# Optimization experiments

Measured on AMD Instinct MI355X. Metric: run time of the kernel, lower is better.

## Reference

```python
import jax, jax.numpy as jnp
import numpy as np

N_NODES = 100000
N_EDGES = 800000
VOCAB = 256      # node_dict_size
NODE_DIM = 256
HIDDEN = 256
N_MASK = 10000


def setup_inputs() -> dict:
    key = jax.random.key(0)
    ks = jax.random.split(key, 8)
    return {
        "x": jax.random.randint(ks[0], (N_NODES, 1), 0, VOCAB, dtype=jnp.int64 if jax.config.jax_enable_x64 else jnp.int32),
        "edge_index": jax.random.randint(ks[1], (2, N_EDGES), 0, N_NODES, dtype=jnp.int32),
        "mask_x_position": jax.random.randint(ks[2], (N_MASK,), 0, N_NODES, dtype=jnp.int32),
        "emb": jax.random.normal(ks[3], (VOCAB, NODE_DIM), dtype=jnp.float32) * (NODE_DIM ** -0.5),
        "W1": jax.random.normal(ks[4], (NODE_DIM, HIDDEN), dtype=jnp.float32) * (NODE_DIM ** -0.5),
        "b1": jnp.zeros((HIDDEN,), dtype=jnp.float32),
        "W2": jax.random.normal(ks[5], (HIDDEN, VOCAB), dtype=jnp.float32) * (HIDDEN ** -0.5),
        "b2": jnp.zeros((VOCAB,), dtype=jnp.float32),
    }


def _gcn_conv(h, W, b, src, dst, norm, n_nodes):
    # PyG GCNConv: out = scatter_add(norm * (h @ W)[src], dst) + b
    hw = h @ W                                      # [N, out]
    msgs = hw[src] * norm[:, None]                  # [E+N, out]
    out = jax.ops.segment_sum(msgs, dst, num_segments=n_nodes)
    return out + b


def _gcn_norm(edge_index, n_nodes):
    # add self-loops, compute sym-normalized edge weights (PyG gcn_norm)
    loops = jnp.arange(n_nodes, dtype=edge_index.dtype)
    src = jnp.concatenate([edge_index[0], loops])
    dst = jnp.concatenate([edge_index[1], loops])
    deg = jax.ops.segment_sum(jnp.ones_like(dst, dtype=jnp.float32), dst,
                              num_segments=n_nodes)  # in-degree incl. self-loop
    dinv = jnp.where(deg > 0, jax.lax.rsqrt(deg), 0.0)
    norm = dinv[src] * dinv[dst]                    # [E+N]
    return src, dst, norm


def reference(x, edge_index, mask_x_position, emb, W1, b1, W2, b2):
    n_nodes = x.shape[0]
    src, dst, norm = _gcn_norm(edge_index, n_nodes)
    h = emb[x[:, 0]]                                # Embedding + squeeze(1) -> [N, node_dim]
    # dropout p=0 / eval mode -> identity
    h = _gcn_conv(h, W1, b1, src, dst, norm, n_nodes)
    h = jax.nn.relu(h)
    h = _gcn_conv(h, W2, b2, src, dst, norm, n_nodes)  # [N, vocab]
    return jax.nn.log_softmax(h[mask_x_position], axis=1)
```

## Files before the change

kernel.cpp:

```cpp
#include <hip/hip_runtime.h>
#include <stdint.h>

#define NN 100000
#define NE 800000
#define ND 256
#define NM 10000
#define NMP 10048
#define NPB 256
#define NBK 391
#define BCAP 2560
#define TILE 4096
#define EBK ((NE + TILE - 1) / TILE)

typedef __attribute__((ext_vector_type(8))) short bf16x8;
typedef __attribute__((ext_vector_type(4))) float f32x4;

__device__ __forceinline__ float bf2f(unsigned short u) {
    return __uint_as_float(((unsigned)u) << 16);
}
__device__ __forceinline__ unsigned short f2bf(float f) {
    unsigned u = __float_as_uint(f);
    u += 0x7fffu + ((u >> 16) & 1u);
    return (unsigned short)(u >> 16);
}


__global__ void k_maskmap(const int* __restrict__ mpos, int* __restrict__ minfo,
                          unsigned char* __restrict__ mb, unsigned char* __restrict__ fb,
                          int* __restrict__ gcur, int* __restrict__ nctr) {
    int j = blockIdx.x * 256 + threadIdx.x;
    if (j < NM) {
        int p = mpos[j];
        minfo[p] = (j + 1) << 1;
        mb[p] = 1;
        fb[p] = 1;
    }
    if (j < NBK) gcur[j << 4] = j * BCAP;
    if (j == 0) *nctr = 0;
}

__global__ __launch_bounds__(256) void k_bin(
    const int* __restrict__ src, const int* __restrict__ dst,
    const unsigned char* __restrict__ mb, unsigned char* __restrict__ fb,
    int* __restrict__ gcur, int* __restrict__ ebuf,
    const float* __restrict__ emb, const float* __restrict__ W1,
    const float* __restrict__ W2,
    unsigned short* __restrict__ M1, unsigned short* __restrict__ W2t) {
    __shared__ int lcnt[NBK];
    __shared__ int sd[TILE], ss[TILE];
    __shared__ float er[ND];
    int b = blockIdx.x, t = threadIdx.x;
    if (b >= EBK) {
        int bb = b - EBK;
        if (bb < ND) {
            er[t] = emb[bb * ND + t];
            __syncthreads();
            float acc = 0.f;
            for (int k = 0; k < ND; k++) acc += er[k] * W1[k * ND + t];
            M1[bb * ND + t] = f2bf(acc);
        } else {
            int n = bb - ND;
            W2t[n * ND + t] = f2bf(W2[t * ND + n]);
        }
        return;
    }
    for (int i = t; i < NBK; i += 256) lcnt[i] = 0;
    __syncthreads();
    int e0 = b * TILE;
#pragma unroll
    for (int k = 0; k < TILE / 256; k++) {
        int idx = t + k * 256;
        int e = e0 + idx;
        if (e < NE) {
            int d = dst[e], s = src[e];
            sd[idx] = d; ss[idx] = s;
            atomicAdd(&lcnt[d >> 8], 1);
            if (mb[d] == 1) fb[s] = 1;
        }
    }
    __syncthreads();
    for (int i = t; i < NBK; i += 256) {
        int c = lcnt[i];
        lcnt[i] = c ? atomicAdd(&gcur[i << 4], c) : 0;
    }
    __syncthreads();
    int nv = min(NE - e0, TILE);
#pragma unroll
    for (int k = 0; k < TILE / 256; k++) {
        int idx = t + k * 256;
        if (idx < nv) {
            int d = sd[idx], s = ss[idx];
            int bk = d >> 8, j = d & 255;
            int pos = atomicAdd(&lcnt[bk], 1);
            if (pos < (bk + 1) * BCAP) ebuf[pos] = s | (j << 17);
        }
    }
}

__global__ void k_bhist(const int* __restrict__ gcur, const int* __restrict__ ebuf,
                        const int* __restrict__ x, const unsigned char* __restrict__ mb,
                        const unsigned char* __restrict__ fb,
                        int* __restrict__ carr, int4* __restrict__ xd4,
                        int* __restrict__ nctr, int* __restrict__ part) {
    __shared__ int bins[NPB];
    __shared__ int rs[4];
    int b = blockIdx.x, t = threadIdx.x;
    int lane = t & 63, wv = t >> 6;
    bins[t] = 0;
    __syncthreads();
    int n = min(gcur[b << 4] - b * BCAP, BCAP);
    int base = b * BCAP;
    for (int i = t; i < n; i += 256)
        atomicAdd(&bins[ebuf[base + i] >> 17], 1);
    __syncthreads();
    int node = b * NPB + t;
    int w = 0;
    if (node < NN) {
        int c = bins[t];
        carr[node] = c;
        float dv = rsqrtf((float)c + 1.0f);
        int cc = 0;
        if (fb[node] == 1) cc = atomicAdd(nctr, 1);
        xd4[node] = make_int4(x[node], __float_as_int(dv), cc, 0);
        w = c + ((mb[node] == 1) ? c : 0);
    }
#pragma unroll
    for (int o = 32; o >= 1; o >>= 1) w += __shfl_xor(w, o, 64);
    if (lane == 0) rs[wv] = w;
    __syncthreads();
    if (t == 0) part[b] = rs[0] + rs[1] + rs[2] + rs[3];
}

__global__ __launch_bounds__(256) void k_place(
    const int* __restrict__ gcur, const int* __restrict__ ebuf,
    const int* __restrict__ minfo, const unsigned char* __restrict__ fb,
    const int* __restrict__ carr, const int* __restrict__ part,
    const int4* __restrict__ xd4, int* __restrict__ off, int2* __restrict__ pairs,
    int4* __restrict__ nrec) {
    __shared__ int sinfo[NPB], lc1[NPB], lc2[NPB];
    __shared__ int bred[4], wtot[4];
    int b = blockIdx.x, t = threadIdx.x;
    int lane = t & 63, wv = t >> 6;
    int pv = 0;
    for (int i = t; i < b; i += 256) pv += part[i];
#pragma unroll
    for (int o = 32; o >= 1; o >>= 1) pv += __shfl_xor(pv, o, 64);
    if (lane == 0) bred[wv] = pv;
    __syncthreads();
    int pbase = bred[0] + bred[1] + bred[2] + bred[3];
    int node = b * NPB + t;
    int c = 0, m = 0, f = 0;
    if (node < NN) {
        c = carr[node];
        int mv = minfo[node];
        if (mv > 0) m = mv;
        f = (fb[node] == 1) ? 1 : 0;
    }
    int wgt = c + (m ? c : 0);
    int xx = wgt;
    for (int o = 1; o < 64; o <<= 1) { int y = __shfl_up(xx, o, 64); if (lane >= o) xx += y; }
    if (lane == 63) wtot[wv] = xx;
    __syncthreads();
    int wadd = 0;
#pragma unroll
    for (int k = 0; k < 4; k++) if (k < wv) wadd += wtot[k];
    int excl = xx - wgt + wadd;
    int myoff = pbase + excl;
    if (node < NN) {
        off[node] = myoff;
        if (f) {
            int4 xv = xd4[node];
            nrec[xv.z] = make_int4(xv.x, xv.y, myoff, c);
        }
    }
    sinfo[t] = m | f;
    lc1[t] = myoff;
    lc2[t] = myoff + c;
    __syncthreads();
    int n = min(gcur[b << 4] - b * BCAP, BCAP);
    int base = b * BCAP;
    for (int i = t; i < n; i += 256) {
        int w = ebuf[base + i];
        int j = w >> 17, s = w & 0x1FFFF;
        int ii = sinfo[j];
        if (ii == 0) continue;
        int4 xv = xd4[s];
        if (ii & 1) {
            int p = atomicAdd(&lc1[j], 1);
            pairs[p] = make_int2(xv.x, xv.y);
        }
        if (ii > 1) {
            int p = atomicAdd(&lc2[j], 1);
            pairs[p] = make_int2(xv.z, xv.y);
        }
    }
}

__global__ __launch_bounds__(1024) void k_expand(
    const int* __restrict__ nctr, const int4* __restrict__ nrec,
    const int2* __restrict__ pairs,
    const unsigned short* __restrict__ M1,
    const float* __restrict__ b1,
    unsigned short* __restrict__ h1c) {
    __shared__ unsigned short sm1[ND * ND];
    int t = threadIdx.x;
    {
        const uint4* g = (const uint4*)M1;
        uint4* s = (uint4*)sm1;
        for (int i = t; i < (ND * ND) / 8; i += 1024) s[i] = g[i];
    }
    __syncthreads();
    int lane = t & 63;
    float4 b1v = ((const float4*)b1)[lane];
    int nw = nctr[0];
    for (int idx = (blockIdx.x * 1024 + t) >> 6; idx < nw; idx += 4096) {
        int4 rec = nrec[idx];
        int v0 = rec.x;
        float w0 = __int_as_float(rec.y);
        ushort4 mm = *(const ushort4*)(sm1 + v0 * ND + lane * 4);
        float a0 = w0 * bf2f(mm.x), a1 = w0 * bf2f(mm.y);
        float a2 = w0 * bf2f(mm.z), a3 = w0 * bf2f(mm.w);
        int e = rec.z, end = e + rec.w;
        for (; e + 4 <= end; e += 4) {
            int2 pA = pairs[e + 0];
            int2 pB = pairs[e + 1];
            int2 pC = pairs[e + 2];
            int2 pD = pairs[e + 3];
            ushort4 mA = *(const ushort4*)(sm1 + pA.x * ND + lane * 4);
            ushort4 mB = *(const ushort4*)(sm1 + pB.x * ND + lane * 4);
            ushort4 mC = *(const ushort4*)(sm1 + pC.x * ND + lane * 4);
            ushort4 mD = *(const ushort4*)(sm1 + pD.x * ND + lane * 4);
            float wA = __int_as_float(pA.y), wB = __int_as_float(pB.y);
            float wC = __int_as_float(pC.y), wD = __int_as_float(pD.y);
            a0 += wA * bf2f(mA.x) + wB * bf2f(mB.x) + wC * bf2f(mC.x) + wD * bf2f(mD.x);
            a1 += wA * bf2f(mA.y) + wB * bf2f(mB.y) + wC * bf2f(mC.y) + wD * bf2f(mD.y);
            a2 += wA * bf2f(mA.z) + wB * bf2f(mB.z) + wC * bf2f(mC.z) + wD * bf2f(mD.z);
            a3 += wA * bf2f(mA.w) + wB * bf2f(mB.w) + wC * bf2f(mC.w) + wD * bf2f(mD.w);
        }
        for (; e < end; e++) {
            int2 p = pairs[e];
            float w = __int_as_float(p.y);
            ushort4 m2 = *(const ushort4*)(sm1 + p.x * ND + lane * 4);
            a0 += w * bf2f(m2.x);
            a1 += w * bf2f(m2.y);
            a2 += w * bf2f(m2.z);
            a3 += w * bf2f(m2.w);
        }
        ushort4 o;
        o.x = f2bf(fmaxf(fmaf(w0, a0, b1v.x), 0.f));
        o.y = f2bf(fmaxf(fmaf(w0, a1, b1v.y), 0.f));
        o.z = f2bf(fmaxf(fmaf(w0, a2, b1v.z), 0.f));
        o.w = f2bf(fmaxf(fmaf(w0, a3, b1v.w), 0.f));
        ((ushort4*)(h1c + (size_t)idx * ND))[lane] = o;
    }
}

__global__ void k_agg2(const int* __restrict__ mpos, const int* __restrict__ minfo,
                       const int4* __restrict__ xd4,
                       const int2* __restrict__ pairs, const int* __restrict__ off,
                       const int* __restrict__ carr,
                       const unsigned short* __restrict__ h1c,
                       unsigned short* __restrict__ agg2b) {
    int lane = threadIdx.x & 63;
    int wave = (blockIdx.x * 256 + threadIdx.x) >> 6;
    if (wave >= NM) return;
    int r = wave;
    int p = mpos[r];
    if ((minfo[p] >> 1) != r + 1) return;
    int4 xp = xd4[p];
    int cp = xp.z;
    float dv = __int_as_float(xp.y);
    ushort4 h0 = *(const ushort4*)(h1c + (size_t)cp * ND + lane * 4);
    float a0 = dv * bf2f(h0.x), a1 = dv * bf2f(h0.y);
    float a2 = dv * bf2f(h0.z), a3 = dv * bf2f(h0.w);
    int c2 = carr[p];
    int e = off[p] + c2, end = e + c2;
    for (; e + 4 <= end; e += 4) {
        int2 pA = pairs[e + 0];
        int2 pB = pairs[e + 1];
        int2 pC = pairs[e + 2];
        int2 pD = pairs[e + 3];
        ushort4 hA = *(const ushort4*)(h1c + (size_t)pA.x * ND + lane * 4);
        ushort4 hB = *(const ushort4*)(h1c + (size_t)pB.x * ND + lane * 4);
        ushort4 hC = *(const ushort4*)(h1c + (size_t)pC.x * ND + lane * 4);
        ushort4 hD = *(const ushort4*)(h1c + (size_t)pD.x * ND + lane * 4);
        float wA = __int_as_float(pA.y), wB = __int_as_float(pB.y);
        float wC = __int_as_float(pC.y), wD = __int_as_float(pD.y);
        a0 += wA * bf2f(hA.x) + wB * bf2f(hB.x) + wC * bf2f(hC.x) + wD * bf2f(hD.x);
        a1 += wA * bf2f(hA.y) + wB * bf2f(hB.y) + wC * bf2f(hC.y) + wD * bf2f(hD.y);
        a2 += wA * bf2f(hA.z) + wB * bf2f(hB.z) + wC * bf2f(hC.z) + wD * bf2f(hD.z);
        a3 += wA * bf2f(hA.w) + wB * bf2f(hB.w) + wC * bf2f(hC.w) + wD * bf2f(hD.w);
    }
    for (; e < end; e++) {
        int2 pp = pairs[e];
        float w = __int_as_float(pp.y);
        ushort4 hv = *(const ushort4*)(h1c + (size_t)pp.x * ND + lane * 4);
        a0 += w * bf2f(hv.x);
        a1 += w * bf2f(hv.y);
        a2 += w * bf2f(hv.z);
        a3 += w * bf2f(hv.w);
    }
    ushort4 o;
    o.x = f2bf(dv * a0);
    o.y = f2bf(dv * a1);
    o.z = f2bf(dv * a2);
    o.w = f2bf(dv * a3);
    ((ushort4*)(agg2b + (size_t)r * ND))[lane] = o;
}

__global__ __launch_bounds__(256) void k_out2(
    const int* __restrict__ mpos, const int* __restrict__ minfo,
    const unsigned short* __restrict__ agg2b, const unsigned short* __restrict__ W2t,
    const float* __restrict__ b2, float* __restrict__ out) {
    int lane = threadIdx.x & 63;
    int wv = threadIdx.x >> 6;
    int row0 = blockIdx.x * 64 + wv * 16;
    int qm = lane & 15, qk = lane >> 4;
    int row = row0 + qm;
    bf16x8 afr[8];
    if (row < NM) {
        int p = mpos[row];
        int rr = (minfo[p] >> 1) - 1;
        const unsigned short* arow = agg2b + (size_t)rr * ND + qk * 8;
#pragma unroll
        for (int kt = 0; kt < 8; kt++) afr[kt] = *(const bf16x8*)(arow + kt * 32);
    } else {
#pragma unroll
        for (int kt = 0; kt < 8; kt++) afr[kt] = (bf16x8){0, 0, 0, 0, 0, 0, 0, 0};
    }
    f32x4 acc[16];
#pragma unroll
    for (int t = 0; t < 16; t++) acc[t] = (f32x4){0.f, 0.f, 0.f, 0.f};
#pragma unroll
    for (int t = 0; t < 16; t++) {
        const unsigned short* brow = W2t + (size_t)(t * 16 + qm) * ND + qk * 8;
#pragma unroll
        for (int kt = 0; kt < 8; kt++) {
            bf16x8 bfr = *(const bf16x8*)(brow + kt * 32);
            acc[t] = __builtin_amdgcn_mfma_f32_16x16x32_bf16(afr[kt], bfr, acc[t], 0, 0, 0);
        }
    }
    float mx[4] = {-1e30f, -1e30f, -1e30f, -1e30f};
#pragma unroll
    for (int t = 0; t < 16; t++) {
        float cb = b2[qm + 16 * t];
#pragma unroll
        for (int r = 0; r < 4; r++) {
            float v = acc[t][r] + cb;
            acc[t][r] = v;
            mx[r] = fmaxf(mx[r], v);
        }
    }
#pragma unroll
    for (int r = 0; r < 4; r++)
        for (int o = 1; o < 16; o <<= 1) mx[r] = fmaxf(mx[r], __shfl_xor(mx[r], o, 64));
    float sm[4] = {0.f, 0.f, 0.f, 0.f};
#pragma unroll
    for (int t = 0; t < 16; t++)
#pragma unroll
        for (int r = 0; r < 4; r++) sm[r] += __expf(acc[t][r] - mx[r]);
#pragma unroll
    for (int r = 0; r < 4; r++)
        for (int o = 1; o < 16; o <<= 1) sm[r] += __shfl_xor(sm[r], o, 64);
#pragma unroll
    for (int r = 0; r < 4; r++) {
        int orow_i = row0 + qk * 4 + r;
        if (orow_i >= NM) continue;
        float lse = mx[r] + __logf(sm[r]);
        float* orow = out + (size_t)orow_i * ND + qm;
#pragma unroll
        for (int t = 0; t < 16; t++) orow[16 * t] = acc[t][r] - lse;
    }
}

extern "C" void kernel_launch(void* const* d_in, const int* in_sizes, int n_in,
                              void* d_out, int out_size, void* d_ws, size_t ws_size,
                              hipStream_t stream) {
    const int* x    = (const int*)d_in[0];
    const int* ei   = (const int*)d_in[1];
    const int* src  = ei;
    const int* dst  = ei + NE;
    const int* mpos = (const int*)d_in[2];
    const float* emb = (const float*)d_in[3];
    const float* W1  = (const float*)d_in[4];
    const float* b1  = (const float*)d_in[5];
    const float* W2  = (const float*)d_in[6];
    const float* b2  = (const float*)d_in[7];
    float* out = (float*)d_out;

    char* w = (char*)d_ws;
    size_t o = 0;
#define ALLOC(nbytes) ({ void* _p = (void*)(w + o); o = (o + (size_t)(nbytes) + 63) & ~(size_t)63; _p; })
    int*   carr  = (int*)ALLOC((size_t)(NN + 64) * 4);
    int*   off   = (int*)ALLOC((size_t)(NN + 64) * 4);
    int*   minfo = (int*)ALLOC((size_t)NN * 4);
    unsigned char* mb = (unsigned char*)ALLOC(NN + 64);
    unsigned char* fb = (unsigned char*)ALLOC(NN + 64);
    int4*  xd4   = (int4*)ALLOC((size_t)NN * 16);
    int*   nctr  = (int*)ALLOC(64);
    int*   part  = (int*)ALLOC(512 * 4);
    int*   gcur  = (int*)ALLOC((size_t)(NBK * 16 + 64) * 4);
    int*   ebuf  = (int*)ALLOC((size_t)NBK * BCAP * 4);
    unsigned short* M1    = (unsigned short*)ALLOC((size_t)ND * ND * 2);
    unsigned short* W2t   = (unsigned short*)ALLOC((size_t)ND * ND * 2);
    unsigned short* agg2b = (unsigned short*)ALLOC((size_t)NM * ND * 2);
    int2*  pairs = (int2*)ALLOC((size_t)NE * 2 * 8);
    int4*  nrec  = (int4*)ALLOC((size_t)NN * 16);
    unsigned short* h1c  = (unsigned short*)ALLOC((size_t)NN * ND * 2);
#undef ALLOC

    k_maskmap<<<(NM + 255) / 256, 256, 0, stream>>>(mpos, minfo, mb, fb, gcur, nctr);
    k_bin<<<EBK + 2 * ND, 256, 0, stream>>>(src, dst, mb, fb, gcur, ebuf,
                                            emb, W1, W2, M1, W2t);
    k_bhist<<<NBK, 256, 0, stream>>>(gcur, ebuf, x, mb, fb, carr, xd4, nctr, part);
    k_place<<<NBK, 256, 0, stream>>>(gcur, ebuf, minfo, fb, carr, part, xd4, off, pairs, nrec);
    k_expand<<<256, 1024, 0, stream>>>(nctr, nrec, pairs, M1, b1, h1c);
    k_agg2<<<(NM + 3) / 4, 256, 0, stream>>>(mpos, minfo, xd4, pairs, off, carr, h1c, agg2b);
    k_out2<<<NMP / 64, 256, 0, stream>>>(mpos, minfo, agg2b, W2t, b2, out);
}
```

Baseline: 190.6 us.

## Merge histogram and placement kernels using global atomic degree counts and atomic offsets

Degree counting moves into the binning kernel as global atomics on carr. The separate histogram and placement kernels become one build kernel that gets each block's base offset from a global atomic counter instead of a prefix over per-block partials. Layer-1 outputs are now indexed by node id and pre-scaled by dinv, so the second aggregation drops per-edge weights and reads a compact per-mask record. This removes one launch and the xd4/off/part arrays, at the cost of 800k global atomics and a nondeterministic edge layout.

```diff
diff --git a/kernel.cpp b/kernel.cpp
--- a/kernel.cpp
+++ b/kernel.cpp
@@ -27,8 +27,10 @@
 
 __global__ void k_maskmap(const int* __restrict__ mpos, int* __restrict__ minfo,
                           unsigned char* __restrict__ mb, unsigned char* __restrict__ fb,
-                          int* __restrict__ gcur, int* __restrict__ nctr) {
+                          int* __restrict__ carr, int* __restrict__ gcur,
+                          int* __restrict__ nctr) {
     int j = blockIdx.x * 256 + threadIdx.x;
+    if (j < NN) carr[j] = 0;
     if (j < NM) {
         int p = mpos[j];
         minfo[p] = (j + 1) << 1;
@@ -36,12 +38,13 @@
         fb[p] = 1;
     }
     if (j < NBK) gcur[j << 4] = j * BCAP;
-    if (j == 0) *nctr = 0;
+    if (j == 0) { nctr[0] = 0; nctr[1] = 0; }
 }
 
 __global__ __launch_bounds__(256) void k_bin(
     const int* __restrict__ src, const int* __restrict__ dst,
     const unsigned char* __restrict__ mb, unsigned char* __restrict__ fb,
+    int* __restrict__ carr,
     int* __restrict__ gcur, int* __restrict__ ebuf,
     const float* __restrict__ emb, const float* __restrict__ W1,
     const float* __restrict__ W2,
@@ -75,6 +78,7 @@
             int d = dst[e], s = src[e];
             sd[idx] = d; ss[idx] = s;
             atomicAdd(&lcnt[d >> 8], 1);
+            atomicAdd(&carr[d], 1);
             if (mb[d] == 1) fb[s] = 1;
         }
     }
@@ -97,101 +101,64 @@
     }
 }
 
-__global__ void k_bhist(const int* __restrict__ gcur, const int* __restrict__ ebuf,
-                        const int* __restrict__ x, const unsigned char* __restrict__ mb,
-                        const unsigned char* __restrict__ fb,
-                        int* __restrict__ carr, int4* __restrict__ xd4,
-                        int* __restrict__ nctr, int* __restrict__ part) {
-    __shared__ int bins[NPB];
-    __shared__ int rs[4];
+__global__ __launch_bounds__(256) void k_build(
+    const int* __restrict__ gcur, const int* __restrict__ ebuf,
+    const int* __restrict__ x, const unsigned char* __restrict__ fb,
+    const int* __restrict__ minfo, const int* __restrict__ carr,
+    int* __restrict__ nctr, int2* __restrict__ pairs,
+    int4* __restrict__ nrec, int4* __restrict__ mrec) {
+    __shared__ int sE[BCAP];
+    __shared__ int sinfo[NPB], lc1[NPB], lc2[NPB];
+    __shared__ int wtot[4];
+    __shared__ int sbase;
     int b = blockIdx.x, t = threadIdx.x;
     int lane = t & 63, wv = t >> 6;
-    bins[t] = 0;
-    __syncthreads();
-    int n = min(gcur[b << 4] - b * BCAP, BCAP);
     int base = b * BCAP;
-    for (int i = t; i < n; i += 256)
-        atomicAdd(&bins[ebuf[base + i] >> 17], 1);
-    __syncthreads();
+    int n = min(gcur[b << 4] - base, BCAP);
+    for (int i = t; i < n; i += 256) sE[i] = ebuf[base + i];
     int node = b * NPB + t;
-    int w = 0;
-    if (node < NN) {
-        int c = bins[t];
-        carr[node] = c;
-        float dv = rsqrtf((float)c + 1.0f);
-        int cc = 0;
-        if (fb[node] == 1) cc = atomicAdd(nctr, 1);
-        xd4[node] = make_int4(x[node], __float_as_int(dv), cc, 0);
-        w = c + ((mb[node] == 1) ? c : 0);
-    }
-#pragma unroll
-    for (int o = 32; o >= 1; o >>= 1) w += __shfl_xor(w, o, 64);
-    if (lane == 0) rs[wv] = w;
-    __syncthreads();
-    if (t == 0) part[b] = rs[0] + rs[1] + rs[2] + rs[3];
-}
-
-__global__ __launch_bounds__(256) void k_place(
-    const int* __restrict__ gcur, const int* __restrict__ ebuf,
-    const int* __restrict__ minfo, const unsigned char* __restrict__ fb,
-    const int* __restrict__ carr, const int* __restrict__ part,
-    const int4* __restrict__ xd4, int* __restrict__ off, int2* __restrict__ pairs,
-    int4* __restrict__ nrec) {
-    __shared__ int sinfo[NPB], lc1[NPB], lc2[NPB];
-    __shared__ int bred[4], wtot[4];
-    int b = blockIdx.x, t = threadIdx.x;
-    int lane = t & 63, wv = t >> 6;
-    int pv = 0;
-    for (int i = t; i < b; i += 256) pv += part[i];
-#pragma unroll
-    for (int o = 32; o >= 1; o >>= 1) pv += __shfl_xor(pv, o, 64);
-    if (lane == 0) bred[wv] = pv;
-    __syncthreads();
-    int pbase = bred[0] + bred[1] + bred[2] + bred[3];
-    int node = b * NPB + t;
-    int c = 0, m = 0, f = 0;
+    int c = 0, m = 0, f = 0, xv = 0;
     if (node < NN) {
         c = carr[node];
+        xv = x[node];
+        if (fb[node] == 1) f = 1;
         int mv = minfo[node];
         if (mv > 0) m = mv;
-        f = (fb[node] == 1) ? 1 : 0;
-    }
-    int wgt = c + (m ? c : 0);
+    }
+    int cc = 0;
+    if (f) cc = atomicAdd(&nctr[0], 1);
+    int wgt = (f ? c : 0) + (m ? c : 0);
     int xx = wgt;
     for (int o = 1; o < 64; o <<= 1) { int y = __shfl_up(xx, o, 64); if (lane >= o) xx += y; }
     if (lane == 63) wtot[wv] = xx;
     __syncthreads();
+    if (t == 0) sbase = atomicAdd(&nctr[1], wtot[0] + wtot[1] + wtot[2] + wtot[3]);
+    __syncthreads();
     int wadd = 0;
 #pragma unroll
     for (int k = 0; k < 4; k++) if (k < wv) wadd += wtot[k];
-    int excl = xx - wgt + wadd;
-    int myoff = pbase + excl;
-    if (node < NN) {
-        off[node] = myoff;
-        if (f) {
-            int4 xv = xd4[node];
-            nrec[xv.z] = make_int4(xv.x, xv.y, myoff, c);
-        }
-    }
+    int myoff = sbase + (xx - wgt) + wadd;
+    float dvf = rsqrtf((float)c + 1.0f);
+    if (f) nrec[cc] = make_int4(xv | (node << 8), __float_as_int(dvf), myoff, c);
+    if (m) mrec[(m >> 1) - 1] = make_int4(myoff + c, __float_as_int(dvf),
+                                          c | (1 << 30), node);
     sinfo[t] = m | f;
     lc1[t] = myoff;
     lc2[t] = myoff + c;
     __syncthreads();
-    int n = min(gcur[b << 4] - b * BCAP, BCAP);
-    int base = b * BCAP;
     for (int i = t; i < n; i += 256) {
-        int w = ebuf[base + i];
+        int w = sE[i];
         int j = w >> 17, s = w & 0x1FFFF;
         int ii = sinfo[j];
         if (ii == 0) continue;
-        int4 xv = xd4[s];
         if (ii & 1) {
+            float ds = rsqrtf((float)carr[s] + 1.0f);
             int p = atomicAdd(&lc1[j], 1);
-            pairs[p] = make_int2(xv.x, xv.y);
+            pairs[p] = make_int2(x[s], __float_as_int(ds));
         }
         if (ii > 1) {
             int p = atomicAdd(&lc2[j], 1);
-            pairs[p] = make_int2(xv.z, xv.y);
+            pairs[p] = make_int2(s, 0);
         }
     }
 }
@@ -215,7 +182,8 @@
     int nw = nctr[0];
     for (int idx = (blockIdx.x * 1024 + t) >> 6; idx < nw; idx += 4096) {
         int4 rec = nrec[idx];
-        int v0 = rec.x;
+        int v0 = rec.x & 255;
+        int nd = ((unsigned)rec.x) >> 8;
         float w0 = __int_as_float(rec.y);
         ushort4 mm = *(const ushort4*)(sm1 + v0 * ND + lane * 4);
         float a0 = w0 * bf2f(mm.x), a1 = w0 * bf2f(mm.y);
@@ -247,58 +215,52 @@
             a3 += w * bf2f(m2.w);
         }
         ushort4 o;
-        o.x = f2bf(fmaxf(fmaf(w0, a0, b1v.x), 0.f));
-        o.y = f2bf(fmaxf(fmaf(w0, a1, b1v.y), 0.f));
-        o.z = f2bf(fmaxf(fmaf(w0, a2, b1v.z), 0.f));
-        o.w = f2bf(fmaxf(fmaf(w0, a3, b1v.w), 0.f));
-        ((ushort4*)(h1c + (size_t)idx * ND))[lane] = o;
-    }
-}
-
-__global__ void k_agg2(const int* __restrict__ mpos, const int* __restrict__ minfo,
-                       const int4* __restrict__ xd4,
-                       const int2* __restrict__ pairs, const int* __restrict__ off,
-                       const int* __restrict__ carr,
+        o.x = f2bf(w0 * fmaxf(fmaf(w0, a0, b1v.x), 0.f));
+        o.y = f2bf(w0 * fmaxf(fmaf(w0, a1, b1v.y), 0.f));
+        o.z = f2bf(w0 * fmaxf(fmaf(w0, a2, b1v.z), 0.f));
+        o.w = f2bf(w0 * fmaxf(fmaf(w0, a3, b1v.w), 0.f));
+        ((ushort4*)(h1c + (size_t)nd * ND))[lane] = o;
+    }
+}
+
+__global__ void k_agg2(const int4* __restrict__ mrec,
+                       const int2* __restrict__ pairs,
                        const unsigned short* __restrict__ h1c,
                        unsigned short* __restrict__ agg2b) {
     int lane = threadIdx.x & 63;
-    int wave = (blockIdx.x * 256 + threadIdx.x) >> 6;
-    if (wave >= NM) return;
-    int r = wave;
-    int p = mpos[r];
-    if ((minfo[p] >> 1) != r + 1) return;
-    int4 xp = xd4[p];
-    int cp = xp.z;
-    float dv = __int_as_float(xp.y);
-    ushort4 h0 = *(const ushort4*)(h1c + (size_t)cp * ND + lane * 4);
-    float a0 = dv * bf2f(h0.x), a1 = dv * bf2f(h0.y);
-    float a2 = dv * bf2f(h0.z), a3 = dv * bf2f(h0.w);
-    int c2 = carr[p];
-    int e = off[p] + c2, end = e + c2;
+    int r = (blockIdx.x * 256 + threadIdx.x) >> 6;
+    if (r >= NM) return;
+    int4 mr = mrec[r];
+    if (!(mr.z & (1 << 30))) return;
+    int e = mr.x;
+    float dv = __int_as_float(mr.y);
+    int c2 = mr.z & 0x3FFFFFFF;
+    int p = mr.w;
+    ushort4 h0 = *(const ushort4*)(h1c + (size_t)p * ND + lane * 4);
+    float a0 = bf2f(h0.x), a1 = bf2f(h0.y);
+    float a2 = bf2f(h0.z), a3 = bf2f(h0.w);
+    int end = e + c2;
     for (; e + 4 <= end; e += 4) {
-        int2 pA = pairs[e + 0];
-        int2 pB = pairs[e + 1];
-        int2 pC = pairs[e + 2];
-        int2 pD = pairs[e + 3];
-        ushort4 hA = *(const ushort4*)(h1c + (size_t)pA.x * ND + lane * 4);
-        ushort4 hB = *(const ushort4*)(h1c + (size_t)pB.x * ND + lane * 4);
-        ushort4 hC = *(const ushort4*)(h1c + (size_t)pC.x * ND + lane * 4);
-        ushort4 hD = *(const ushort4*)(h1c + (size_t)pD.x * ND + lane * 4);
-        float wA = __int_as_float(pA.y), wB = __int_as_float(pB.y);
-        float wC = __int_as_float(pC.y), wD = __int_as_float(pD.y);
-        a0 += wA * bf2f(hA.x) + wB * bf2f(hB.x) + wC * bf2f(hC.x) + wD * bf2f(hD.x);
-        a1 += wA * bf2f(hA.y) + wB * bf2f(hB.y) + wC * bf2f(hC.y) + wD * bf2f(hD.y);
-        a2 += wA * bf2f(hA.z) + wB * bf2f(hB.z) + wC * bf2f(hC.z) + wD * bf2f(hD.z);
-        a3 += wA * bf2f(hA.w) + wB * bf2f(hB.w) + wC * bf2f(hC.w) + wD * bf2f(hD.w);
+        int sA = pairs[e + 0].x;
+        int sB = pairs[e + 1].x;
+        int sC = pairs[e + 2].x;
+        int sD = pairs[e + 3].x;
+        ushort4 hA = *(const ushort4*)(h1c + (size_t)sA * ND + lane * 4);
+        ushort4 hB = *(const ushort4*)(h1c + (size_t)sB * ND + lane * 4);
+        ushort4 hC = *(const ushort4*)(h1c + (size_t)sC * ND + lane * 4);
+        ushort4 hD = *(const ushort4*)(h1c + (size_t)sD * ND + lane * 4);
+        a0 += bf2f(hA.x) + bf2f(hB.x) + bf2f(hC.x) + bf2f(hD.x);
+        a1 += bf2f(hA.y) + bf2f(hB.y) + bf2f(hC.y) + bf2f(hD.y);
+        a2 += bf2f(hA.z) + bf2f(hB.z) + bf2f(hC.z) + bf2f(hD.z);
+        a3 += bf2f(hA.w) + bf2f(hB.w) + bf2f(hC.w) + bf2f(hD.w);
     }
     for (; e < end; e++) {
-        int2 pp = pairs[e];
-        float w = __int_as_float(pp.y);
-        ushort4 hv = *(const ushort4*)(h1c + (size_t)pp.x * ND + lane * 4);
-        a0 += w * bf2f(hv.x);
-        a1 += w * bf2f(hv.y);
-        a2 += w * bf2f(hv.z);
-        a3 += w * bf2f(hv.w);
+        int s = pairs[e].x;
+        ushort4 hv = *(const ushort4*)(h1c + (size_t)s * ND + lane * 4);
+        a0 += bf2f(hv.x);
+        a1 += bf2f(hv.y);
+        a2 += bf2f(hv.z);
+        a3 += bf2f(hv.w);
     }
     ushort4 o;
     o.x = f2bf(dv * a0);
@@ -392,13 +354,10 @@
     size_t o = 0;
 #define ALLOC(nbytes) ({ void* _p = (void*)(w + o); o = (o + (size_t)(nbytes) + 63) & ~(size_t)63; _p; })
     int*   carr  = (int*)ALLOC((size_t)(NN + 64) * 4);
-    int*   off   = (int*)ALLOC((size_t)(NN + 64) * 4);
     int*   minfo = (int*)ALLOC((size_t)NN * 4);
     unsigned char* mb = (unsigned char*)ALLOC(NN + 64);
     unsigned char* fb = (unsigned char*)ALLOC(NN + 64);
-    int4*  xd4   = (int4*)ALLOC((size_t)NN * 16);
     int*   nctr  = (int*)ALLOC(64);
-    int*   part  = (int*)ALLOC(512 * 4);
     int*   gcur  = (int*)ALLOC((size_t)(NBK * 16 + 64) * 4);
     int*   ebuf  = (int*)ALLOC((size_t)NBK * BCAP * 4);
     unsigned short* M1    = (unsigned short*)ALLOC((size_t)ND * ND * 2);
@@ -406,15 +365,16 @@
     unsigned short* agg2b = (unsigned short*)ALLOC((size_t)NM * ND * 2);
     int2*  pairs = (int2*)ALLOC((size_t)NE * 2 * 8);
     int4*  nrec  = (int4*)ALLOC((size_t)NN * 16);
+    int4*  mrec  = (int4*)ALLOC((size_t)NM * 16);
     unsigned short* h1c  = (unsigned short*)ALLOC((size_t)NN * ND * 2);
 #undef ALLOC
 
-    k_maskmap<<<(NM + 255) / 256, 256, 0, stream>>>(mpos, minfo, mb, fb, gcur, nctr);
-    k_bin<<<EBK + 2 * ND, 256, 0, stream>>>(src, dst, mb, fb, gcur, ebuf,
+    k_maskmap<<<(NN + 255) / 256, 256, 0, stream>>>(mpos, minfo, mb, fb, carr, gcur, nctr);
+    k_bin<<<EBK + 2 * ND, 256, 0, stream>>>(src, dst, mb, fb, carr, gcur, ebuf,
                                             emb, W1, W2, M1, W2t);
-    k_bhist<<<NBK, 256, 0, stream>>>(gcur, ebuf, x, mb, fb, carr, xd4, nctr, part);
-    k_place<<<NBK, 256, 0, stream>>>(gcur, ebuf, minfo, fb, carr, part, xd4, off, pairs, nrec);
+    k_build<<<NBK, 256, 0, stream>>>(gcur, ebuf, x, fb, minfo, carr,
+                                     nctr, pairs, nrec, mrec);
     k_expand<<<256, 1024, 0, stream>>>(nctr, nrec, pairs, M1, b1, h1c);
-    k_agg2<<<(NM + 3) / 4, 256, 0, stream>>>(mpos, minfo, xd4, pairs, off, carr, h1c, agg2b);
+    k_agg2<<<(NM + 3) / 4, 256, 0, stream>>>(mrec, pairs, h1c, agg2b);
     k_out2<<<NMP / 64, 256, 0, stream>>>(mpos, minfo, agg2b, W2t, b2, out);
 }
```

After: 208.7 us. 1.09x slower.

## Pack edge pairs into 32-bit words and count degrees with global atomics

Applied to the files above, without the earlier changes.

Each edge pair record shrinks from an int2 (index plus float weight) to one int that packs the index in the high bits and the in-degree, clamped to 255, in the low 8 bits. The weight is recomputed with rsqrtf in the aggregation loops. Degree counting moves from a per-bucket shared histogram pass in a separate kernel into global atomics inside k_bin, so the histogram kernel becomes a simple per-node pass. This halves pair-array traffic at the cost of extra rsqrt work, global atomic contention, and wrong weights for any node with in-degree above 255.

```diff
diff --git a/kernel.cpp b/kernel.cpp
--- a/kernel.cpp
+++ b/kernel.cpp
@@ -27,8 +27,10 @@
 
 __global__ void k_maskmap(const int* __restrict__ mpos, int* __restrict__ minfo,
                           unsigned char* __restrict__ mb, unsigned char* __restrict__ fb,
-                          int* __restrict__ gcur, int* __restrict__ nctr) {
+                          int* __restrict__ carr, int* __restrict__ gcur,
+                          int* __restrict__ nctr) {
     int j = blockIdx.x * 256 + threadIdx.x;
+    if (j < NN) carr[j] = 0;
     if (j < NM) {
         int p = mpos[j];
         minfo[p] = (j + 1) << 1;
@@ -42,6 +44,7 @@
 __global__ __launch_bounds__(256) void k_bin(
     const int* __restrict__ src, const int* __restrict__ dst,
     const unsigned char* __restrict__ mb, unsigned char* __restrict__ fb,
+    int* __restrict__ carr,
     int* __restrict__ gcur, int* __restrict__ ebuf,
     const float* __restrict__ emb, const float* __restrict__ W1,
     const float* __restrict__ W2,
@@ -75,6 +78,7 @@
             int d = dst[e], s = src[e];
             sd[idx] = d; ss[idx] = s;
             atomicAdd(&lcnt[d >> 8], 1);
+            atomicAdd(&carr[d], 1);
             if (mb[d] == 1) fb[s] = 1;
         }
     }
@@ -97,31 +101,21 @@
     }
 }
 
-__global__ void k_bhist(const int* __restrict__ gcur, const int* __restrict__ ebuf,
-                        const int* __restrict__ x, const unsigned char* __restrict__ mb,
-                        const unsigned char* __restrict__ fb,
-                        int* __restrict__ carr, int4* __restrict__ xd4,
-                        int* __restrict__ nctr, int* __restrict__ part) {
-    __shared__ int bins[NPB];
+__global__ __launch_bounds__(256) void k_nodes(
+    const int* __restrict__ x, const unsigned char* __restrict__ mb,
+    const unsigned char* __restrict__ fb, const int* __restrict__ carr,
+    int4* __restrict__ xd4, int* __restrict__ nctr, int* __restrict__ part) {
     __shared__ int rs[4];
     int b = blockIdx.x, t = threadIdx.x;
     int lane = t & 63, wv = t >> 6;
-    bins[t] = 0;
-    __syncthreads();
-    int n = min(gcur[b << 4] - b * BCAP, BCAP);
-    int base = b * BCAP;
-    for (int i = t; i < n; i += 256)
-        atomicAdd(&bins[ebuf[base + i] >> 17], 1);
-    __syncthreads();
     int node = b * NPB + t;
     int w = 0;
     if (node < NN) {
-        int c = bins[t];
-        carr[node] = c;
+        int c = carr[node];
         float dv = rsqrtf((float)c + 1.0f);
         int cc = 0;
         if (fb[node] == 1) cc = atomicAdd(nctr, 1);
-        xd4[node] = make_int4(x[node], __float_as_int(dv), cc, 0);
+        xd4[node] = make_int4(x[node], __float_as_int(dv), cc, min(c, 255));
         w = c + ((mb[node] == 1) ? c : 0);
     }
 #pragma unroll
@@ -135,7 +129,7 @@
     const int* __restrict__ gcur, const int* __restrict__ ebuf,
     const int* __restrict__ minfo, const unsigned char* __restrict__ fb,
     const int* __restrict__ carr, const int* __restrict__ part,
-    const int4* __restrict__ xd4, int* __restrict__ off, int2* __restrict__ pairs,
+    const int4* __restrict__ xd4, int* __restrict__ off, int* __restrict__ pairs,
     int4* __restrict__ nrec) {
     __shared__ int sinfo[NPB], lc1[NPB], lc2[NPB];
     __shared__ int bred[4], wtot[4];
@@ -187,18 +181,18 @@
         int4 xv = xd4[s];
         if (ii & 1) {
             int p = atomicAdd(&lc1[j], 1);
-            pairs[p] = make_int2(xv.x, xv.y);
+            pairs[p] = (xv.x << 8) | xv.w;
         }
         if (ii > 1) {
             int p = atomicAdd(&lc2[j], 1);
-            pairs[p] = make_int2(xv.z, xv.y);
+            pairs[p] = (xv.z << 8) | xv.w;
         }
     }
 }
 
 __global__ __launch_bounds__(1024) void k_expand(
     const int* __restrict__ nctr, const int4* __restrict__ nrec,
-    const int2* __restrict__ pairs,
+    const int* __restrict__ pairs,
     const unsigned short* __restrict__ M1,
     const float* __restrict__ b1,
     unsigned short* __restrict__ h1c) {
@@ -222,25 +216,27 @@
         float a2 = w0 * bf2f(mm.z), a3 = w0 * bf2f(mm.w);
         int e = rec.z, end = e + rec.w;
         for (; e + 4 <= end; e += 4) {
-            int2 pA = pairs[e + 0];
-            int2 pB = pairs[e + 1];
-            int2 pC = pairs[e + 2];
-            int2 pD = pairs[e + 3];
-            ushort4 mA = *(const ushort4*)(sm1 + pA.x * ND + lane * 4);
-            ushort4 mB = *(const ushort4*)(sm1 + pB.x * ND + lane * 4);
-            ushort4 mC = *(const ushort4*)(sm1 + pC.x * ND + lane * 4);
-            ushort4 mD = *(const ushort4*)(sm1 + pD.x * ND + lane * 4);
-            float wA = __int_as_float(pA.y), wB = __int_as_float(pB.y);
-            float wC = __int_as_float(pC.y), wD = __int_as_float(pD.y);
+            int pA = pairs[e + 0];
+            int pB = pairs[e + 1];
+            int pC = pairs[e + 2];
+            int pD = pairs[e + 3];
+            ushort4 mA = *(const ushort4*)(sm1 + (pA >> 8) * ND + lane * 4);
+            ushort4 mB = *(const ushort4*)(sm1 + (pB >> 8) * ND + lane * 4);
+            ushort4 mC = *(const ushort4*)(sm1 + (pC >> 8) * ND + lane * 4);
+            ushort4 mD = *(const ushort4*)(sm1 + (pD >> 8) * ND + lane * 4);
+            float wA = rsqrtf((float)(pA & 255) + 1.0f);
+            float wB = rsqrtf((float)(pB & 255) + 1.0f);
+            float wC = rsqrtf((float)(pC & 255) + 1.0f);
+            float wD = rsqrtf((float)(pD & 255) + 1.0f);
             a0 += wA * bf2f(mA.x) + wB * bf2f(mB.x) + wC * bf2f(mC.x) + wD * bf2f(mD.x);
             a1 += wA * bf2f(mA.y) + wB * bf2f(mB.y) + wC * bf2f(mC.y) + wD * bf2f(mD.y);
             a2 += wA * bf2f(mA.z) + wB * bf2f(mB.z) + wC * bf2f(mC.z) + wD * bf2f(mD.z);
             a3 += wA * bf2f(mA.w) + wB * bf2f(mB.w) + wC * bf2f(mC.w) + wD * bf2f(mD.w);
         }
         for (; e < end; e++) {
-            int2 p = pairs[e];
-            float w = __int_as_float(p.y);
-            ushort4 m2 = *(const ushort4*)(sm1 + p.x * ND + lane * 4);
+            int p = pairs[e];
+            float w = rsqrtf((float)(p & 255) + 1.0f);
+            ushort4 m2 = *(const ushort4*)(sm1 + (p >> 8) * ND + lane * 4);
             a0 += w * bf2f(m2.x);
             a1 += w * bf2f(m2.y);
             a2 += w * bf2f(m2.z);
@@ -257,7 +253,7 @@
 
 __global__ void k_agg2(const int* __restrict__ mpos, const int* __restrict__ minfo,
                        const int4* __restrict__ xd4,
-                       const int2* __restrict__ pairs, const int* __restrict__ off,
+                       const int* __restrict__ pairs, const int* __restrict__ off,
                        const int* __restrict__ carr,
                        const unsigned short* __restrict__ h1c,
                        unsigned short* __restrict__ agg2b) {
@@ -276,25 +272,27 @@
     int c2 = carr[p];
     int e = off[p] + c2, end = e + c2;
     for (; e + 4 <= end; e += 4) {
-        int2 pA = pairs[e + 0];
-        int2 pB = pairs[e + 1];
-        int2 pC = pairs[e + 2];
-        int2 pD = pairs[e + 3];
-        ushort4 hA = *(const ushort4*)(h1c + (size_t)pA.x * ND + lane * 4);
-        ushort4 hB = *(const ushort4*)(h1c + (size_t)pB.x * ND + lane * 4);
-        ushort4 hC = *(const ushort4*)(h1c + (size_t)pC.x * ND + lane * 4);
-        ushort4 hD = *(const ushort4*)(h1c + (size_t)pD.x * ND + lane * 4);
-        float wA = __int_as_float(pA.y), wB = __int_as_float(pB.y);
-        float wC = __int_as_float(pC.y), wD = __int_as_float(pD.y);
+        int pA = pairs[e + 0];
+        int pB = pairs[e + 1];
+        int pC = pairs[e + 2];
+        int pD = pairs[e + 3];
+        ushort4 hA = *(const ushort4*)(h1c + (size_t)(pA >> 8) * ND + lane * 4);
+        ushort4 hB = *(const ushort4*)(h1c + (size_t)(pB >> 8) * ND + lane * 4);
+        ushort4 hC = *(const ushort4*)(h1c + (size_t)(pC >> 8) * ND + lane * 4);
+        ushort4 hD = *(const ushort4*)(h1c + (size_t)(pD >> 8) * ND + lane * 4);
+        float wA = rsqrtf((float)(pA & 255) + 1.0f);
+        float wB = rsqrtf((float)(pB & 255) + 1.0f);
+        float wC = rsqrtf((float)(pC & 255) + 1.0f);
+        float wD = rsqrtf((float)(pD & 255) + 1.0f);
         a0 += wA * bf2f(hA.x) + wB * bf2f(hB.x) + wC * bf2f(hC.x) + wD * bf2f(hD.x);
         a1 += wA * bf2f(hA.y) + wB * bf2f(hB.y) + wC * bf2f(hC.y) + wD * bf2f(hD.y);
         a2 += wA * bf2f(hA.z) + wB * bf2f(hB.z) + wC * bf2f(hC.z) + wD * bf2f(hD.z);
         a3 += wA * bf2f(hA.w) + wB * bf2f(hB.w) + wC * bf2f(hC.w) + wD * bf2f(hD.w);
     }
     for (; e < end; e++) {
-        int2 pp = pairs[e];
-        float w = __int_as_float(pp.y);
-        ushort4 hv = *(const ushort4*)(h1c + (size_t)pp.x * ND + lane * 4);
+        int pp = pairs[e];
+        float w = rsqrtf((float)(pp & 255) + 1.0f);
+        ushort4 hv = *(const ushort4*)(h1c + (size_t)(pp >> 8) * ND + lane * 4);
         a0 += w * bf2f(hv.x);
         a1 += w * bf2f(hv.y);
         a2 += w * bf2f(hv.z);
@@ -404,15 +402,15 @@
     unsigned short* M1    = (unsigned short*)ALLOC((size_t)ND * ND * 2);
     unsigned short* W2t   = (unsigned short*)ALLOC((size_t)ND * ND * 2);
     unsigned short* agg2b = (unsigned short*)ALLOC((size_t)NM * ND * 2);
-    int2*  pairs = (int2*)ALLOC((size_t)NE * 2 * 8);
+    int*   pairs = (int*)ALLOC((size_t)NE * 2 * 4);
     int4*  nrec  = (int4*)ALLOC((size_t)NN * 16);
     unsigned short* h1c  = (unsigned short*)ALLOC((size_t)NN * ND * 2);
 #undef ALLOC
 
-    k_maskmap<<<(NM + 255) / 256, 256, 0, stream>>>(mpos, minfo, mb, fb, gcur, nctr);
-    k_bin<<<EBK + 2 * ND, 256, 0, stream>>>(src, dst, mb, fb, gcur, ebuf,
+    k_maskmap<<<(NN + 255) / 256, 256, 0, stream>>>(mpos, minfo, mb, fb, carr, gcur, nctr);
+    k_bin<<<EBK + 2 * ND, 256, 0, stream>>>(src, dst, mb, fb, carr, gcur, ebuf,
                                             emb, W1, W2, M1, W2t);
-    k_bhist<<<NBK, 256, 0, stream>>>(gcur, ebuf, x, mb, fb, carr, xd4, nctr, part);
+    k_nodes<<<NBK, 256, 0, stream>>>(x, mb, fb, carr, xd4, nctr, part);
     k_place<<<NBK, 256, 0, stream>>>(gcur, ebuf, minfo, fb, carr, part, xd4, off, pairs, nrec);
     k_expand<<<256, 1024, 0, stream>>>(nctr, nrec, pairs, M1, b1, h1c);
     k_agg2<<<(NM + 3) / 4, 256, 0, stream>>>(mpos, minfo, xd4, pairs, off, carr, h1c, agg2b);
```

After: 212.4 us. +11.5%, slower.
